# Performance work log

Hardware: AMD Instinct MI355X
Metric: run time of the kernel (lower is better)

Reference implementation:

```python
import jax, jax.numpy as jnp
import numpy as np

X_DIM = [128, 256, 512]
IMG_H, IMG_W = 105, 105
T = 1000
DT, TAU = 0.01, 1.0
K = 32
P_MIN = 1e-16


def setup_inputs() -> dict:
    key = jax.random.key(0)
    ks = jax.random.split(key, 12)

    def rn(k, shape, scale=1.0):
        return jax.random.normal(k, shape, jnp.float32) * scale

    # binary image with one 'on' pixel -> initial pen position via argwhere
    data = jnp.zeros((IMG_H, IMG_W), bool).at[52, 52].set(True)
    return {
        'data': data,
        'z1': jax.random.uniform(ks[0], (K,), jnp.float32),          # top-layer alphas
        'z2': rn(ks[1], (X_DIM[0],)),                                 # top-layer init state
        'gamma': jax.random.uniform(ks[2], (3,), jnp.float32, 0.3, 0.7),
        'pen_log_var': jnp.array(2.0, jnp.float32),
        'W_a0': rn(ks[3], (K, X_DIM[0]), X_DIM[0] ** -0.5),
        'W_a1': rn(ks[4], (K, X_DIM[1]), X_DIM[1] ** -0.5),
        'b_a0': jnp.zeros((K,), jnp.float32),
        'b_a1': jnp.zeros((K,), jnp.float32),
        'W_u0': rn(ks[5], (X_DIM[1], X_DIM[0]), X_DIM[0] ** -0.5),
        'W_u1': rn(ks[6], (X_DIM[2], X_DIM[1]), X_DIM[1] ** -0.5),
        'W_p': rn(ks[7], (3, X_DIM[2]), X_DIM[2] ** -0.5),
        'b_p': jnp.zeros((3,), jnp.float32),
        # attractor dynamics matrices, scaled for stable Euler integration
        'A0': rn(ks[8], (K, X_DIM[0], X_DIM[0]), 0.5 * X_DIM[0] ** -0.5),
        'A1': rn(ks[9], (K, X_DIM[1], X_DIM[1]), 0.5 * X_DIM[1] ** -0.5),
        'A2': rn(ks[10], (K, X_DIM[2], X_DIM[2]), 0.5 * X_DIM[2] ** -0.5),
    }


def _decode(data, z1, z2, gamma, pen_log_var, W_a0, W_a1, b_a0, b_a1,
            W_u0, W_u1, W_p, b_p, A0, A1, A2):
    grid_x = jnp.linspace(0.5, IMG_W - 0.5, IMG_W)
    grid_y = jnp.linspace(0.5, IMG_H - 0.5, IMG_H)
    img_dims = jnp.array([IMG_H, IMG_W], jnp.float32)
    # stabilise_variance: lower-bound the variance
    log_var = jnp.log(jnp.exp(pen_log_var) + P_MIN)
    inv_var = jnp.exp(-log_var)

    def step(carry, z1_t):
        x, pen_xy = carry
        alphas = [z1_t,
                  jax.nn.softmax(W_a0 @ x[0] + b_a0, axis=0),
                  jax.nn.softmax(W_a1 @ x[1] + b_a1, axis=0)]
        u = [jnp.zeros_like(x[0]), W_u0 @ x[0], W_u1 @ x[1]]

        def upd(A, g, xl, al, ul):
            aAx = jnp.einsum('k,kij,j->i', al, A, xl)  # alpha-weighted attractor drive
            return xl + ((1 - g) * aAx - g * xl + ul) * (DT / TAU)

        x_new = [upd(A0, gamma[0], x[0], alphas[0], u[0]),
                 upd(A1, gamma[1], x[1], alphas[1], u[1]),
                 upd(A2, gamma[2], x[2], alphas[2], u[2])]
        pen_actions = W_p @ x_new[2] + b_p
        d_xy = pen_actions[:2]
        pen_down_log_p = jax.nn.log_sigmoid(pen_actions[2])
        # per-pixel Bernoulli parameter: separable Gaussian kernel on the grid
        ll_y = -0.5 * (pen_xy[0] - grid_y) ** 2 * inv_var
        ll_x = -0.5 * (pen_xy[1] - grid_x) ** 2 * inv_var
        p_xy = jnp.exp(ll_y[:, None] + ll_x[None, :] + pen_down_log_p)
        p_xy = p_xy * (1 - 2 * P_MIN) + P_MIN  # stabilise_cross_entropy
        # pen position update with sigmoid squashing to the image
        pen = pen_xy + d_xy
        pen = jax.nn.sigmoid((pen - img_dims / 2) * 4 / img_dims) * img_dims
        return (x_new, pen), (alphas, u, x_new, pen, p_xy, pen_down_log_p)

    x0 = [z2, jnp.zeros((X_DIM[1],), jnp.float32), jnp.zeros((X_DIM[2],), jnp.float32)]
    pen_xy0 = jnp.argwhere(data, size=1)[0].astype(jnp.float32)
    inputs = jnp.broadcast_to(z1[None, :], (T, K))
    _, (alphas, u, x, pen_xy, p_xy_t, pen_down_log_p) = jax.lax.scan(step, (x0, pen_xy0), inputs)
    return (*alphas, *u, *x, pen_xy, p_xy_t, pen_down_log_p)


def reference(data, z1, z2, gamma, pen_log_var, W_a0, W_a1, b_a0, b_a1,
              W_u0, W_u1, W_p, b_p, A0, A1, A2):
    return _decode(data, z1, z2, gamma, pen_log_var, W_a0, W_a1, b_a0, b_a1,
                   W_u0, W_u1, W_p, b_p, A0, A1, A2)
```

## Files before the change

### kernel.cpp

```cpp
#include <hip/hip_runtime.h>
#include <math.h>

#define T_STEPS 1000
#define KK 32
#define D0 128
#define D1 256
#define D2 512
#define IMGH 105
#define IMGW 105
#define NPIX (IMGH*IMGW)
#define DTTAU 0.01f

#define NB 256
#define NT 512

typedef unsigned long long ull;

#define OFF_M0   0
#define OFF_PX0  16384
#define OFF_PX1  16896
#define OFF_PX2  17920
#define OFF_S2T  19968
#define OFF_PA   531968
#define OFF_PXYP 534968
#define OFF_PENS 537968

#define OA0  0
#define OA1  32000
#define OA2  64000
#define OU0  96000
#define OU1  224000
#define OU2  480000
#define OX0  992000
#define OX1  1120000
#define OX2  1376000
#define OPEN 1888000
#define OPXY 1890000
#define OPDLP 12915000

#define DOT4(a,b) ((a).x*(b).x + (a).y*(b).y + (a).z*(b).z + (a).w*(b).w)

__device__ __forceinline__ float waveReduceSum(float v) {
    for (int m = 32; m >= 1; m >>= 1) v += __shfl_xor(v, m, 64);
    return v;
}
__device__ __forceinline__ ull packPair(float v, unsigned stamp) {
    return ((ull)stamp << 32) | (ull)__float_as_uint(v);
}

__global__ __launch_bounds__(256) void setup_kernel(
    const void* __restrict__ dataRaw, const float* __restrict__ z2,
    float* __restrict__ ws)
{
    if (blockIdx.x != 0) return;
    int tid = threadIdx.x;
    ull* PX0 = (ull*)(ws + OFF_PX0);
    ull* PX1 = (ull*)(ws + OFF_PX1);
    ull* PX2 = (ull*)(ws + OFF_PX2);
    const ull INVALID = 0xFFFFFFFF00000000ULL;

    if (tid < D0) { PX0[tid] = packPair(z2[tid], 0); PX0[D0 + tid] = INVALID; }
    if (tid < D1) { PX1[tid] = packPair(0.f, 0);     PX1[D1 + tid] = INVALID; }
    for (int i = tid; i < D2; i += 256) { PX2[i] = packPair(0.f, 0); PX2[D2 + i] = INVALID; }

    __shared__ int sMin;
    if (tid == 0) sMin = 0x7fffffff;
    __syncthreads();
    const unsigned char* db = (const unsigned char*)dataRaw;
    for (int i = tid; i < NPIX; i += 256) if (db[i]) atomicMin(&sMin, i);
    __syncthreads();
    if (sMin == 0x7fffffff) {
        const int* di = (const int*)dataRaw;
        for (int i = tid; i < NPIX; i += 256) if (di[i] != 0) atomicMin(&sMin, i);
    }
    __syncthreads();
    if (tid == 0) {
        int idx = (sMin == 0x7fffffff) ? 0 : sMin;
        (ws + OFF_PENS)[0] = (float)(idx / IMGW);
        (ws + OFF_PENS)[1] = (float)(idx % IMGW);
    }
}

__global__ __launch_bounds__(256) void m0_kernel(
    const float* __restrict__ z1, const float* __restrict__ A0, float* __restrict__ ws)
{
    int idx = blockIdx.x * 256 + threadIdx.x;
    if (idx < D0 * D0) {
        float s = 0.f;
        for (int k = 0; k < KK; k++) s += z1[k] * A0[(size_t)k * D0 * D0 + idx];
        ws[OFF_M0 + idx] = s;
    }
}

__global__ __launch_bounds__(256) void fill_kernel(const float* __restrict__ z1, float* __restrict__ out)
{
    size_t gid = (size_t)blockIdx.x * blockDim.x + threadIdx.x;
    size_t nthr = (size_t)gridDim.x * blockDim.x;
    for (size_t i = gid; i < 32000; i += nthr) out[OA0 + i] = z1[i & 31];
    for (size_t i = gid; i < 128000; i += nthr) out[OU0 + i] = 0.f;
}

__global__ __launch_bounds__(NT, 2) void persist_kernel(
    const float* __restrict__ A1, const float* __restrict__ A2,
    const float* __restrict__ Wu0, const float* __restrict__ Wu1,
    const float* __restrict__ Wa0, const float* __restrict__ Wa1,
    const float* __restrict__ ba0, const float* __restrict__ ba1,
    const float* __restrict__ Wp, const float* __restrict__ bp,
    const float* __restrict__ gam,
    float* __restrict__ ws, float* __restrict__ out)
{
    const int b = blockIdx.x;
    const int tid = threadIdx.x;
    const int lane = tid & 63;
    const int w = tid >> 6;
    const int k = tid >> 4;
    const int c = tid & 15;

    float4 a2r0[8], a2r1[8], a1r[4];
    {
        const float4* p0 = (const float4*)(A2 + ((size_t)k * D2 + 2 * b) * D2 + c * 32);
        const float4* p1 = (const float4*)(A2 + ((size_t)k * D2 + 2 * b + 1) * D2 + c * 32);
        #pragma unroll
        for (int jj = 0; jj < 8; ++jj) { a2r0[jj] = p0[jj]; a2r1[jj] = p1[jj]; }
        const float4* p2 = (const float4*)(A1 + ((size_t)k * D1 + b) * D1 + c * 16);
        #pragma unroll
        for (int jj = 0; jj < 4; ++jj) a1r[jj] = p2[jj];
    }
    const float g0 = gam[0], g1 = gam[1], g2 = gam[2];

    __shared__ __align__(16) float x0s[D0];
    __shared__ __align__(16) float x1s[16 * 20];
    __shared__ __align__(16) float x2s[16 * 36];
    __shared__ float pre[64];
    __shared__ float red2a[KK], red2b[KK], red1[KK];
    __shared__ float uS[3];

    ull* PX0 = (ull*)(ws + OFF_PX0);
    ull* PX1 = (ull*)(ws + OFF_PX1);
    ull* PX2 = (ull*)(ws + OFF_PX2);

    const int hasB1 = (tid < 256);
    const int hasB0 = (tid >= 256 && tid < 384);

    #pragma unroll 1
    for (int t = 0; t < T_STEPS; ++t) {
        const int p = t & 1;
        const unsigned want = (unsigned)t;

        {
            ull pa_ = 0, pb_ = 0;
            bool okA = false, okB = !(hasB1 || hasB0);
            ull* srcB = hasB1 ? &PX1[p * D1 + tid]
                              : (hasB0 ? &PX0[p * D0 + (tid - 256)] : (ull*)0);
            do {
                if (!okA) {
                    pa_ = __hip_atomic_load(&PX2[p * D2 + tid], __ATOMIC_RELAXED, __HIP_MEMORY_SCOPE_AGENT);
                    okA = ((unsigned)(pa_ >> 32) == want);
                }
                if (!okB) {
                    pb_ = __hip_atomic_load(srcB, __ATOMIC_RELAXED, __HIP_MEMORY_SCOPE_AGENT);
                    okB = ((unsigned)(pb_ >> 32) == want);
                }
            } while (!(okA && okB));
            x2s[(tid >> 5) * 36 + (tid & 31)] = __uint_as_float((unsigned)pa_);
            if (hasB1) x1s[(tid >> 4) * 20 + (tid & 15)] = __uint_as_float((unsigned)pb_);
            else if (hasB0) x0s[tid - 256] = __uint_as_float((unsigned)pb_);
        }
        __syncthreads();

        {
            float s = 0.f;
            const float4* wr = (const float4*)(Wa1 + (size_t)k * D1 + c * 16);
            const float4* xc = (const float4*)(x1s + c * 20);
            #pragma unroll
            for (int jj = 0; jj < 4; ++jj) { float4 a = wr[jj], x = xc[jj]; s += DOT4(a, x); }
            s += __shfl_xor(s, 1, 64); s += __shfl_xor(s, 2, 64);
            s += __shfl_xor(s, 4, 64); s += __shfl_xor(s, 8, 64);
            if (c == 0) pre[k] = s + ba1[k];

            float s1 = 0.f;
            const float4* wr1 = (const float4*)(Wa0 + (size_t)k * D0 + c * 8);
            const float4* xc1 = (const float4*)(x0s + c * 8);
            #pragma unroll
            for (int jj = 0; jj < 2; ++jj) { float4 a = wr1[jj], x = xc1[jj]; s1 += DOT4(a, x); }
            s1 += __shfl_xor(s1, 1, 64); s1 += __shfl_xor(s1, 2, 64);
            s1 += __shfl_xor(s1, 4, 64); s1 += __shfl_xor(s1, 8, 64);
            if (c == 0) pre[32 + k] = s1 + ba0[k];

            const float4* x24 = (const float4*)x2s;
            float sa = 0.f, sb = 0.f;
            #pragma unroll
            for (int jj = 0; jj < 8; ++jj) {
                float4 x = x24[c * 9 + jj];
                sa += DOT4(a2r0[jj], x);
                sb += DOT4(a2r1[jj], x);
            }
            sa += __shfl_xor(sa, 1, 64); sa += __shfl_xor(sa, 2, 64);
            sa += __shfl_xor(sa, 4, 64); sa += __shfl_xor(sa, 8, 64);
            sb += __shfl_xor(sb, 1, 64); sb += __shfl_xor(sb, 2, 64);
            sb += __shfl_xor(sb, 4, 64); sb += __shfl_xor(sb, 8, 64);
            const float4* x14 = (const float4*)x1s;
            float sc = 0.f;
            #pragma unroll
            for (int jj = 0; jj < 4; ++jj) {
                float4 x = x14[c * 5 + jj];
                sc += DOT4(a1r[jj], x);
            }
            sc += __shfl_xor(sc, 1, 64); sc += __shfl_xor(sc, 2, 64);
            sc += __shfl_xor(sc, 4, 64); sc += __shfl_xor(sc, 8, 64);
            if (c == 0) { red2a[k] = sa; red2b[k] = sb; red1[k] = sc; }
        }
        if (w == 1 && t > 0) {
            const float4* x24 = (const float4*)x2s;
            #pragma unroll
            for (int r = 0; r < 3; ++r) {
                const float4* wr = (const float4*)(Wp + (size_t)r * D2);
                float s = 0.f;
                #pragma unroll
                for (int it = 0; it < 2; ++it) {
                    int e4 = lane + 64 * it;
                    float4 x = x24[(e4 >> 3) * 9 + (e4 & 7)];
                    float4 a = wr[e4];
                    s += DOT4(a, x);
                }
                s = waveReduceSum(s);
                if (lane == 0) {
                    if (r < 2) ws[OFF_PA + (size_t)(t - 1) * 3 + r] = s + bp[r];
                    else {
                        float z = s + bp[2];
                        float pdlp = fminf(z, 0.f) - log1pf(expf(-fabsf(z)));
                        ws[OFF_PA + (size_t)(t - 1) * 3 + 2] = pdlp;
                        out[OPDLP + (t - 1)] = pdlp;
                    }
                }
            }
        } else if (w == 4 || w == 5) {
            int eg = 2 * b + (w - 4);
            const float4* wr = (const float4*)(Wu1 + (size_t)eg * D1);
            const float4* x4 = (const float4*)x1s;
            float4 a = wr[lane];
            float4 x = x4[(lane >> 2) * 5 + (lane & 3)];
            float s = DOT4(a, x);
            s = waveReduceSum(s);
            if (lane == 0) { uS[w - 4] = s; out[OU2 + (size_t)t * D2 + eg] = s; }
        } else if (w == 6) {
            float s = 0.f;
            if (lane < 32) {
                const float4* wr = (const float4*)(Wu0 + (size_t)b * D0);
                const float4* x4 = (const float4*)x0s;
                float4 a = wr[lane], x = x4[lane];
                s = DOT4(a, x);
            }
            s = waveReduceSum(s);
            if (lane == 0) { uS[2] = s; out[OU1 + (size_t)t * D1 + b] = s; }
        } else if (w == 7 && b < D0) {
            float s = 0.f;
            if (lane < 32) {
                const float4* mr = (const float4*)(ws + OFF_M0 + (size_t)b * D0);
                const float4* x4 = (const float4*)x0s;
                float4 a = mr[lane], x = x4[lane];
                s = DOT4(a, x);
            }
            s = waveReduceSum(s);
            if (lane == 0) {
                float xo = x0s[b];
                float xn = xo + ((1.f - g0) * s - g0 * xo) * DTTAU;
                __hip_atomic_store(&PX0[(p ^ 1) * D0 + b], packPair(xn, (unsigned)(t + 1)),
                                   __ATOMIC_RELAXED, __HIP_MEMORY_SCOPE_AGENT);
                out[OX0 + (size_t)t * D0 + b] = xn;
            }
        }
        __syncthreads();

        if (w == 0) {
            float pv = pre[lane];
            float m = pv;
            m = fmaxf(m, __shfl_xor(m, 16, 64)); m = fmaxf(m, __shfl_xor(m, 8, 64));
            m = fmaxf(m, __shfl_xor(m, 4, 64));  m = fmaxf(m, __shfl_xor(m, 2, 64));
            m = fmaxf(m, __shfl_xor(m, 1, 64));
            float e = expf(pv - m);
            float ss = e;
            ss += __shfl_xor(ss, 16, 64); ss += __shfl_xor(ss, 8, 64);
            ss += __shfl_xor(ss, 4, 64);  ss += __shfl_xor(ss, 2, 64); ss += __shfl_xor(ss, 1, 64);
            float al = e / ss;
            if (b == 0) {
                if (lane < 32) out[OA2 + (size_t)t * KK + lane] = al;
                else           out[OA1 + (size_t)t * KK + (lane - 32)] = al;
            }
            float r1 = (lane < 32) ? red2a[lane] : red1[lane - 32];
            float r2 = (lane < 32) ? red2b[lane] : 0.f;
            float v1 = al * r1, v2 = al * r2;
            v1 += __shfl_xor(v1, 16, 64); v1 += __shfl_xor(v1, 8, 64);
            v1 += __shfl_xor(v1, 4, 64);  v1 += __shfl_xor(v1, 2, 64); v1 += __shfl_xor(v1, 1, 64);
            v2 += __shfl_xor(v2, 16, 64); v2 += __shfl_xor(v2, 8, 64);
            v2 += __shfl_xor(v2, 4, 64);  v2 += __shfl_xor(v2, 2, 64); v2 += __shfl_xor(v2, 1, 64);
            if (lane == 0) {
                int eg = 2 * b;
                float xo0 = x2s[(eg >> 5) * 36 + (eg & 31)];
                float xn0 = xo0 + ((1.f - g2) * v1 - g2 * xo0 + uS[0]) * DTTAU;
                __hip_atomic_store(&PX2[(p ^ 1) * D2 + eg], packPair(xn0, (unsigned)(t + 1)),
                                   __ATOMIC_RELAXED, __HIP_MEMORY_SCOPE_AGENT);
                out[OX2 + (size_t)t * D2 + eg] = xn0;
                int eh = eg + 1;
                float xo1 = x2s[(eh >> 5) * 36 + (eh & 31)];
                float xn1 = xo1 + ((1.f - g2) * v2 - g2 * xo1 + uS[1]) * DTTAU;
                __hip_atomic_store(&PX2[(p ^ 1) * D2 + eh], packPair(xn1, (unsigned)(t + 1)),
                                   __ATOMIC_RELAXED, __HIP_MEMORY_SCOPE_AGENT);
                out[OX2 + (size_t)t * D2 + eh] = xn1;
                if (t == T_STEPS - 1) {
                    ws[OFF_S2T + (size_t)t * D2 + eg] = xn0;
                    ws[OFF_S2T + (size_t)t * D2 + eh] = xn1;
                }
            }
            if (lane == 32) {
                float xo = x1s[(b >> 4) * 20 + (b & 15)];
                float xn = xo + ((1.f - g1) * v1 - g1 * xo + uS[2]) * DTTAU;
                __hip_atomic_store(&PX1[(p ^ 1) * D1 + b], packPair(xn, (unsigned)(t + 1)),
                                   __ATOMIC_RELAXED, __HIP_MEMORY_SCOPE_AGENT);
                out[OX1 + (size_t)t * D1 + b] = xn;
            }
        }
        __syncthreads();
    }
}

__global__ __launch_bounds__(192) void chain_kernel(
    const float* __restrict__ Wp, const float* __restrict__ bp,
    float* __restrict__ ws, float* __restrict__ out)
{
    int tid = threadIdx.x;
    int w = tid >> 6, lane = tid & 63;
    {
        const float4* x2 = (const float4*)(ws + OFF_S2T + (size_t)(T_STEPS - 1) * D2);
        const float4* wr = (const float4*)(Wp + (size_t)w * D2);
        float p = 0.f;
        #pragma unroll
        for (int it = 0; it < 2; ++it) {
            float4 a = wr[lane + 64 * it], x = x2[lane + 64 * it];
            p += DOT4(a, x);
        }
        p = waveReduceSum(p);
        if (lane == 0) {
            if (w < 2) ws[OFF_PA + (size_t)(T_STEPS - 1) * 3 + w] = p + bp[w];
            else {
                float z = p + bp[2];
                float pdlp = fminf(z, 0.f) - log1pf(expf(-fabsf(z)));
                ws[OFF_PA + (size_t)(T_STEPS - 1) * 3 + 2] = pdlp;
                out[OPDLP + (T_STEPS - 1)] = pdlp;
            }
        }
    }
    __syncthreads();
    if (tid != 0) return;
    float py = ws[OFF_PENS], px = ws[OFF_PENS + 1];
    for (int t = 0; t < T_STEPS; ++t) {
        float dy = ws[OFF_PA + t * 3], dx = ws[OFF_PA + t * 3 + 1], pdlp = ws[OFF_PA + t * 3 + 2];
        ws[OFF_PXYP + t * 3] = py; ws[OFF_PXYP + t * 3 + 1] = px; ws[OFF_PXYP + t * 3 + 2] = pdlp;
        float ny = py + dy, nx = px + dx;
        ny = 105.f / (1.f + expf(-(ny - 52.5f) * (4.f / 105.f)));
        nx = 105.f / (1.f + expf(-(nx - 52.5f) * (4.f / 105.f)));
        py = ny; px = nx;
        out[OPEN + (size_t)t * 2] = py;
        out[OPEN + (size_t)t * 2 + 1] = px;
    }
}

__global__ __launch_bounds__(256) void pxy_kernel(
    const float* __restrict__ plv, const float* __restrict__ ws, float* __restrict__ out)
{
    int t = blockIdx.x;
    const float* pxyp = ws + OFF_PXYP + (size_t)t * 3;
    float py = pxyp[0], px = pxyp[1], pdlp = pxyp[2];
    float inv_var = 1.0f / (expf(plv[0]) + 1e-16f);
    for (int p = threadIdx.x; p < NPIX; p += 256) {
        int i = p / IMGW, j = p % IMGW;
        float ddy = py - ((float)i + 0.5f);
        float ddx = px - ((float)j + 0.5f);
        float v = expf(-0.5f * inv_var * (ddy * ddy + ddx * ddx) + pdlp);
        out[OPXY + (size_t)t * NPIX + p] = v + 1e-16f;
    }
}

extern "C" void kernel_launch(void* const* d_in, const int* in_sizes, int n_in,
                              void* d_out, int out_size, void* d_ws, size_t ws_size,
                              hipStream_t stream)
{
    const void*  data = d_in[0];
    const float* z1  = (const float*)d_in[1];
    const float* z2  = (const float*)d_in[2];
    const float* gam = (const float*)d_in[3];
    const float* plv = (const float*)d_in[4];
    const float* Wa0 = (const float*)d_in[5];
    const float* Wa1 = (const float*)d_in[6];
    const float* ba0 = (const float*)d_in[7];
    const float* ba1 = (const float*)d_in[8];
    const float* Wu0 = (const float*)d_in[9];
    const float* Wu1 = (const float*)d_in[10];
    const float* Wp  = (const float*)d_in[11];
    const float* bp  = (const float*)d_in[12];
    const float* A0  = (const float*)d_in[13];
    const float* A1  = (const float*)d_in[14];
    const float* A2  = (const float*)d_in[15];
    float* out = (float*)d_out;
    float* ws  = (float*)d_ws;

    hipLaunchKernelGGL(setup_kernel, dim3(1), dim3(256), 0, stream, data, z2, ws);
    hipLaunchKernelGGL(m0_kernel, dim3(64), dim3(256), 0, stream, z1, A0, ws);
    hipLaunchKernelGGL(fill_kernel, dim3(128), dim3(256), 0, stream, z1, out);
    hipLaunchKernelGGL(persist_kernel, dim3(NB), dim3(NT), 0, stream,
                       A1, A2, Wu0, Wu1, Wa0, Wa1, ba0, ba1, Wp, bp, gam, ws, out);
    hipLaunchKernelGGL(chain_kernel, dim3(1), dim3(192), 0, stream, Wp, bp, ws, out);
    hipLaunchKernelGGL(pxy_kernel, dim3(T_STEPS), dim3(256), 0, stream, plv, ws, out);
}
```

Before: 6.066 ms.

## Replace per-element stamped values with per-block step flags for grid sync

Each state value used to carry a timestamp that every consumer polled. Now each block publishes one step flag after waiting for its state stores to complete, and a single wave polls all 256 flags with a backoff sleep before the block reads plain values. Layer-2 pairs are packed into one 64-bit store, and output stores are moved after the flag publish so they stay off the critical path. The risk is memory-ordering correctness: relaxed atomics plus s_waitcnt are used in place of stamp validation, and the layer-0 store is not covered by the waitcnt in the w==0 branch.

```diff
diff --git a/kernel.cpp b/kernel.cpp
--- a/kernel.cpp
+++ b/kernel.cpp
@@ -24,6 +24,7 @@
 #define OFF_PA   531968
 #define OFF_PXYP 534968
 #define OFF_PENS 537968
+#define OFF_FLG  538112
 
 #define OA0  0
 #define OA1  32000
@@ -44,9 +45,6 @@
     for (int m = 32; m >= 1; m >>= 1) v += __shfl_xor(v, m, 64);
     return v;
 }
-__device__ __forceinline__ ull packPair(float v, unsigned stamp) {
-    return ((ull)stamp << 32) | (ull)__float_as_uint(v);
-}
 
 __global__ __launch_bounds__(256) void setup_kernel(
     const void* __restrict__ dataRaw, const float* __restrict__ z2,
@@ -54,14 +52,11 @@
 {
     if (blockIdx.x != 0) return;
     int tid = threadIdx.x;
-    ull* PX0 = (ull*)(ws + OFF_PX0);
-    ull* PX1 = (ull*)(ws + OFF_PX1);
-    ull* PX2 = (ull*)(ws + OFF_PX2);
-    const ull INVALID = 0xFFFFFFFF00000000ULL;
-
-    if (tid < D0) { PX0[tid] = packPair(z2[tid], 0); PX0[D0 + tid] = INVALID; }
-    if (tid < D1) { PX1[tid] = packPair(0.f, 0);     PX1[D1 + tid] = INVALID; }
-    for (int i = tid; i < D2; i += 256) { PX2[i] = packPair(0.f, 0); PX2[D2 + i] = INVALID; }
+
+    if (tid < D0) (ws + OFF_PX0)[tid] = z2[tid];
+    (ws + OFF_PX1)[tid] = 0.f;
+    for (int i = tid; i < D2; i += 256) (ws + OFF_PX2)[i] = 0.f;
+    ((int*)(ws + OFF_FLG))[tid] = 0;
 
     __shared__ int sMin;
     if (tid == 0) sMin = 0x7fffffff;
@@ -135,36 +130,42 @@
     __shared__ float red2a[KK], red2b[KK], red1[KK];
     __shared__ float uS[3];
 
-    ull* PX0 = (ull*)(ws + OFF_PX0);
-    ull* PX1 = (ull*)(ws + OFF_PX1);
-    ull* PX2 = (ull*)(ws + OFF_PX2);
-
-    const int hasB1 = (tid < 256);
-    const int hasB0 = (tid >= 256 && tid < 384);
+    float* PX0 = ws + OFF_PX0;
+    float* PX1 = ws + OFF_PX1;
+    ull*   PX2 = (ull*)(ws + OFF_PX2);
+    int*   FLG = (int*)(ws + OFF_FLG);
 
     #pragma unroll 1
     for (int t = 0; t < T_STEPS; ++t) {
         const int p = t & 1;
-        const unsigned want = (unsigned)t;
-
-        {
-            ull pa_ = 0, pb_ = 0;
-            bool okA = false, okB = !(hasB1 || hasB0);
-            ull* srcB = hasB1 ? &PX1[p * D1 + tid]
-                              : (hasB0 ? &PX0[p * D0 + (tid - 256)] : (ull*)0);
-            do {
-                if (!okA) {
-                    pa_ = __hip_atomic_load(&PX2[p * D2 + tid], __ATOMIC_RELAXED, __HIP_MEMORY_SCOPE_AGENT);
-                    okA = ((unsigned)(pa_ >> 32) == want);
-                }
-                if (!okB) {
-                    pb_ = __hip_atomic_load(srcB, __ATOMIC_RELAXED, __HIP_MEMORY_SCOPE_AGENT);
-                    okB = ((unsigned)(pb_ >> 32) == want);
-                }
-            } while (!(okA && okB));
-            x2s[(tid >> 5) * 36 + (tid & 31)] = __uint_as_float((unsigned)pa_);
-            if (hasB1) x1s[(tid >> 4) * 20 + (tid & 15)] = __uint_as_float((unsigned)pb_);
-            else if (hasB0) x0s[tid - 256] = __uint_as_float((unsigned)pb_);
+
+        if (w == 0 && t > 0) {
+            for (;;) {
+                int f0 = __hip_atomic_load(FLG + lane,       __ATOMIC_RELAXED, __HIP_MEMORY_SCOPE_AGENT);
+                int f1 = __hip_atomic_load(FLG + 64 + lane,  __ATOMIC_RELAXED, __HIP_MEMORY_SCOPE_AGENT);
+                int f2 = __hip_atomic_load(FLG + 128 + lane, __ATOMIC_RELAXED, __HIP_MEMORY_SCOPE_AGENT);
+                int f3 = __hip_atomic_load(FLG + 192 + lane, __ATOMIC_RELAXED, __HIP_MEMORY_SCOPE_AGENT);
+                int m = min(min(f0, f1), min(f2, f3));
+                for (int msk = 32; msk >= 1; msk >>= 1) m = min(m, __shfl_xor(m, msk, 64));
+                if (m >= t) break;
+                __builtin_amdgcn_s_sleep(1);
+            }
+        }
+        __syncthreads();
+
+        if (tid < 256) {
+            ull v = __hip_atomic_load(&PX2[p * 256 + tid], __ATOMIC_RELAXED, __HIP_MEMORY_SCOPE_AGENT);
+            int e = 2 * tid;
+            x2s[(e >> 5) * 36 + (e & 31)]       = __uint_as_float((unsigned)v);
+            x2s[((e+1) >> 5) * 36 + ((e+1)&31)] = __uint_as_float((unsigned)(v >> 32));
+        } else {
+            int i = tid - 256;
+            float v1 = __hip_atomic_load(&PX1[p * D1 + i], __ATOMIC_RELAXED, __HIP_MEMORY_SCOPE_AGENT);
+            x1s[(i >> 4) * 20 + (i & 15)] = v1;
+            if (i < D0) {
+                float v0 = __hip_atomic_load(&PX0[p * D0 + i], __ATOMIC_RELAXED, __HIP_MEMORY_SCOPE_AGENT);
+                x0s[i] = v0;
+            }
         }
         __syncthreads();
 
@@ -265,8 +266,7 @@
             if (lane == 0) {
                 float xo = x0s[b];
                 float xn = xo + ((1.f - g0) * s - g0 * xo) * DTTAU;
-                __hip_atomic_store(&PX0[(p ^ 1) * D0 + b], packPair(xn, (unsigned)(t + 1)),
-                                   __ATOMIC_RELAXED, __HIP_MEMORY_SCOPE_AGENT);
+                __hip_atomic_store(&PX0[(p ^ 1) * D0 + b], xn, __ATOMIC_RELAXED, __HIP_MEMORY_SCOPE_AGENT);
                 out[OX0 + (size_t)t * D0 + b] = xn;
             }
         }
@@ -283,10 +283,6 @@
             ss += __shfl_xor(ss, 16, 64); ss += __shfl_xor(ss, 8, 64);
             ss += __shfl_xor(ss, 4, 64);  ss += __shfl_xor(ss, 2, 64); ss += __shfl_xor(ss, 1, 64);
             float al = e / ss;
-            if (b == 0) {
-                if (lane < 32) out[OA2 + (size_t)t * KK + lane] = al;
-                else           out[OA1 + (size_t)t * KK + (lane - 32)] = al;
-            }
             float r1 = (lane < 32) ? red2a[lane] : red1[lane - 32];
             float r2 = (lane < 32) ? red2b[lane] : 0.f;
             float v1 = al * r1, v2 = al * r2;
@@ -294,31 +290,42 @@
             v1 += __shfl_xor(v1, 4, 64);  v1 += __shfl_xor(v1, 2, 64); v1 += __shfl_xor(v1, 1, 64);
             v2 += __shfl_xor(v2, 16, 64); v2 += __shfl_xor(v2, 8, 64);
             v2 += __shfl_xor(v2, 4, 64);  v2 += __shfl_xor(v2, 2, 64); v2 += __shfl_xor(v2, 1, 64);
+
+            float xn0 = 0.f, xn1 = 0.f, xnl1 = 0.f;
             if (lane == 0) {
                 int eg = 2 * b;
                 float xo0 = x2s[(eg >> 5) * 36 + (eg & 31)];
-                float xn0 = xo0 + ((1.f - g2) * v1 - g2 * xo0 + uS[0]) * DTTAU;
-                __hip_atomic_store(&PX2[(p ^ 1) * D2 + eg], packPair(xn0, (unsigned)(t + 1)),
-                                   __ATOMIC_RELAXED, __HIP_MEMORY_SCOPE_AGENT);
-                out[OX2 + (size_t)t * D2 + eg] = xn0;
+                xn0 = xo0 + ((1.f - g2) * v1 - g2 * xo0 + uS[0]) * DTTAU;
                 int eh = eg + 1;
                 float xo1 = x2s[(eh >> 5) * 36 + (eh & 31)];
-                float xn1 = xo1 + ((1.f - g2) * v2 - g2 * xo1 + uS[1]) * DTTAU;
-                __hip_atomic_store(&PX2[(p ^ 1) * D2 + eh], packPair(xn1, (unsigned)(t + 1)),
-                                   __ATOMIC_RELAXED, __HIP_MEMORY_SCOPE_AGENT);
-                out[OX2 + (size_t)t * D2 + eh] = xn1;
+                xn1 = xo1 + ((1.f - g2) * v2 - g2 * xo1 + uS[1]) * DTTAU;
+                ull pack = ((ull)__float_as_uint(xn1) << 32) | (ull)__float_as_uint(xn0);
+                __hip_atomic_store(&PX2[(p ^ 1) * 256 + b], pack, __ATOMIC_RELAXED, __HIP_MEMORY_SCOPE_AGENT);
+            }
+            if (lane == 32) {
+                float xo = x1s[(b >> 4) * 20 + (b & 15)];
+                xnl1 = xo + ((1.f - g1) * v1 - g1 * xo + uS[2]) * DTTAU;
+                __hip_atomic_store(&PX1[(p ^ 1) * D1 + b], xnl1, __ATOMIC_RELAXED, __HIP_MEMORY_SCOPE_AGENT);
+            }
+            if (t < T_STEPS - 1) {
+                asm volatile("s_waitcnt vmcnt(0)" ::: "memory");
+                if (lane == 0)
+                    __hip_atomic_store(FLG + b, t + 1, __ATOMIC_RELAXED, __HIP_MEMORY_SCOPE_AGENT);
+            }
+            if (b == 0) {
+                if (lane < 32) out[OA2 + (size_t)t * KK + lane] = al;
+                else           out[OA1 + (size_t)t * KK + (lane - 32)] = al;
+            }
+            if (lane == 0) {
+                int eg = 2 * b;
+                out[OX2 + (size_t)t * D2 + eg] = xn0;
+                out[OX2 + (size_t)t * D2 + eg + 1] = xn1;
                 if (t == T_STEPS - 1) {
                     ws[OFF_S2T + (size_t)t * D2 + eg] = xn0;
-                    ws[OFF_S2T + (size_t)t * D2 + eh] = xn1;
+                    ws[OFF_S2T + (size_t)t * D2 + eg + 1] = xn1;
                 }
             }
-            if (lane == 32) {
-                float xo = x1s[(b >> 4) * 20 + (b & 15)];
-                float xn = xo + ((1.f - g1) * v1 - g1 * xo + uS[2]) * DTTAU;
-                __hip_atomic_store(&PX1[(p ^ 1) * D1 + b], packPair(xn, (unsigned)(t + 1)),
-                                   __ATOMIC_RELAXED, __HIP_MEMORY_SCOPE_AGENT);
-                out[OX1 + (size_t)t * D1 + b] = xn;
-            }
+            if (lane == 32) out[OX1 + (size_t)t * D1 + b] = xnl1;
         }
         __syncthreads();
     }
```

After: 8.004 ms. 31.9% more time.
